# Kernel tuning notes

Measured on AMD Instinct MI355X. Metric: run time of the kernel, lower is better.

Reference implementation:

```python
import jax, jax.numpy as jnp
import numpy as np

B, T, D, H = 256, 256, 64, 512  # batch, seq_len, input_dim, hidden_dim


def setup_inputs() -> dict:
    key = jax.random.key(0)
    ks = jax.random.split(key, 12)
    scale = 0.05
    inp = {"x": jax.random.normal(ks[0], (B, T, D), dtype=jnp.float32)}
    in_dims = [D, H, H]
    for i in range(3):
        inp[f"Wx{i}"] = jax.random.normal(ks[1 + 3 * i], (in_dims[i], H), dtype=jnp.float32) * scale
        inp[f"Wh{i}"] = jax.random.normal(ks[2 + 3 * i], (H, H), dtype=jnp.float32) * scale
        inp[f"b{i}"] = jnp.zeros((H,), dtype=jnp.float32)
    inp["Wf"] = jax.random.normal(ks[10], (H, 1), dtype=jnp.float32) * scale
    inp["bf"] = jnp.zeros((1,), dtype=jnp.float32)
    return inp


def _rnn_seq(x, Wx, Wh, b):
    """SimpleRNN with return_sequences=True. x: [B,T,Din] -> [B,T,H].
    Keras eval mode: dropout inactive. h_t = tanh(x_t Wx + h_{t-1} Wh + b)."""
    # Precompute input projection for all steps (one big GEMM).
    xp = jnp.einsum('btd,dh->bth', x, Wx) + b  # [B,T,H]

    def step(h, xt):
        h2 = jnp.tanh(xt + h @ Wh)
        return h2, h2

    h0 = jnp.zeros((x.shape[0], Wh.shape[0]), dtype=x.dtype)
    _, ys = jax.lax.scan(step, h0, jnp.swapaxes(xp, 0, 1))  # ys: [T,B,H]
    return jnp.swapaxes(ys, 0, 1)


def _rnn_last(x, Wx, Wh, b):
    """SimpleRNN with return_sequences=False. x: [B,T,Din] -> [B,H] (final state)."""
    xp = jnp.einsum('btd,dh->bth', x, Wx) + b

    def step(h, xt):
        h2 = jnp.tanh(xt + h @ Wh)
        return h2, None

    h0 = jnp.zeros((x.shape[0], Wh.shape[0]), dtype=x.dtype)
    hT, _ = jax.lax.scan(step, h0, jnp.swapaxes(xp, 0, 1))
    return hT


def reference(x, Wx0, Wh0, b0, Wx1, Wh1, b1, Wx2, Wh2, b2, Wf, bf):
    h = _rnn_seq(x, Wx0, Wh0, b0)   # [B,T,H]
    h = _rnn_seq(h, Wx1, Wh1, b1)   # [B,T,H]
    h = _rnn_last(h, Wx2, Wh2, b2)  # [B,H]
    return h @ Wf + bf              # [B,1]
```

## Files before the change

### kernel.cpp

```cpp
#include <hip/hip_runtime.h>


typedef unsigned short u16;
typedef unsigned int   u32;

typedef __attribute__((ext_vector_type(8))) short short8;
typedef __attribute__((ext_vector_type(4))) float f32x4;
typedef __attribute__((ext_vector_type(4))) int   i32x4;

#define N_B 256
#define N_T 256
#define N_D 64
#define N_H 512
#define LAY 3
#define BG  8
#define CGS 8
#define ROWS 32
#define WCOL 64
#define CNT_TGT 8
#define HSK_TGT 24
#define CPAD 16
#define CNT_LINES (LAY * BG * N_T)
#define CNT_U32   ((CNT_LINES + 2 * BG) * CPAD)
#define SPIN_LIM (1u << 22)

__device__ __forceinline__ u16 f2bf(float f) {
  union { float f; u32 u; } v; v.f = f;
  u32 u = v.u;
  u += 0x7fffu + ((u >> 16) & 1u);
  return (u16)(u >> 16);
}
__device__ __forceinline__ float bf2f(u16 h) {
  union { u32 u; float f; } v; v.u = ((u32)h) << 16;
  return v.f;
}
__device__ __forceinline__ short8 ld8(const u16* p) { return *(const short8*)p; }
__device__ __forceinline__ short8 cvt8(const float* p) {
  short8 r;
#pragma unroll
  for (int j = 0; j < 8; ++j) r[j] = (short)f2bf(p[j]);
  return r;
}
__device__ __forceinline__ short8 as_s8(i32x4 v) {
  union { i32x4 i; short8 s; } u; u.i = v; return u.s;
}
__device__ __forceinline__ float fast_tanh(float x) {
  float xc = fminf(fmaxf(x, -9.f), 9.f);
  float e  = __builtin_amdgcn_exp2f(xc * 2.8853900817779268f);
  return 1.f - 2.f * __builtin_amdgcn_rcpf(e + 1.f);
}
__device__ __forceinline__ u32 rmw_read(u32* p) {
  u32 v, z = 0;
  asm volatile("global_atomic_add %0, %1, %2, off sc0\n\ts_waitcnt vmcnt(0)"
               : "=v"(v) : "v"(p), "v"(z) : "memory");
  return v;
}
__device__ __forceinline__ void poll_cnt(u32* cp, u32 target, bool fast, bool* dead) {
  u32 it = 0;
  for (;;) {
    u32 v = fast ? rmw_read(cp)
                 : __hip_atomic_load(cp, __ATOMIC_RELAXED, __HIP_MEMORY_SCOPE_AGENT);
    if (v >= target) return;
    if (it >= 2) __builtin_amdgcn_s_sleep(1);
    if (++it > SPIN_LIM) { *dead = true; return; }
  }
}
__device__ __forceinline__ void lds_set(volatile u32* f, u32 v) {
  __hip_atomic_store((u32*)f, v, __ATOMIC_RELEASE, __HIP_MEMORY_SCOPE_WORKGROUP);
}
__device__ __forceinline__ void lds_wait(volatile u32* f, u32 want, bool* dead) {
  u32 it = 0;
  while (__hip_atomic_load((u32*)f, __ATOMIC_ACQUIRE, __HIP_MEMORY_SCOPE_WORKGROUP) != want) {
    if (++it > SPIN_LIM) { *dead = true; return; }
  }
}

__device__ __forceinline__ void load_frags16_fast(const u16* p, i32x4 f[16]) {
  asm volatile(
      "global_load_dwordx4 %0, %16, off sc0\n\t"
      "global_load_dwordx4 %1, %16, off offset:64 sc0\n\t"
      "global_load_dwordx4 %2, %16, off offset:128 sc0\n\t"
      "global_load_dwordx4 %3, %16, off offset:192 sc0\n\t"
      "global_load_dwordx4 %4, %16, off offset:256 sc0\n\t"
      "global_load_dwordx4 %5, %16, off offset:320 sc0\n\t"
      "global_load_dwordx4 %6, %16, off offset:384 sc0\n\t"
      "global_load_dwordx4 %7, %16, off offset:448 sc0\n\t"
      "global_load_dwordx4 %8, %16, off offset:512 sc0\n\t"
      "global_load_dwordx4 %9, %16, off offset:576 sc0\n\t"
      "global_load_dwordx4 %10, %16, off offset:640 sc0\n\t"
      "global_load_dwordx4 %11, %16, off offset:704 sc0\n\t"
      "global_load_dwordx4 %12, %16, off offset:768 sc0\n\t"
      "global_load_dwordx4 %13, %16, off offset:832 sc0\n\t"
      "global_load_dwordx4 %14, %16, off offset:896 sc0\n\t"
      "global_load_dwordx4 %15, %16, off offset:960 sc0\n\t"
      "s_waitcnt vmcnt(0)"
      : "=&v"(f[0]), "=&v"(f[1]), "=&v"(f[2]), "=&v"(f[3]),
        "=&v"(f[4]), "=&v"(f[5]), "=&v"(f[6]), "=&v"(f[7]),
        "=&v"(f[8]), "=&v"(f[9]), "=&v"(f[10]), "=&v"(f[11]),
        "=&v"(f[12]), "=&v"(f[13]), "=&v"(f[14]), "=&v"(f[15])
      : "v"(p) : "memory");
}
__device__ __forceinline__ void load_frags16_slow(const u16* p, i32x4 f[16]) {
  asm volatile(
      "global_load_dwordx4 %0, %16, off sc0 sc1\n\t"
      "global_load_dwordx4 %1, %16, off offset:64 sc0 sc1\n\t"
      "global_load_dwordx4 %2, %16, off offset:128 sc0 sc1\n\t"
      "global_load_dwordx4 %3, %16, off offset:192 sc0 sc1\n\t"
      "global_load_dwordx4 %4, %16, off offset:256 sc0 sc1\n\t"
      "global_load_dwordx4 %5, %16, off offset:320 sc0 sc1\n\t"
      "global_load_dwordx4 %6, %16, off offset:384 sc0 sc1\n\t"
      "global_load_dwordx4 %7, %16, off offset:448 sc0 sc1\n\t"
      "global_load_dwordx4 %8, %16, off offset:512 sc0 sc1\n\t"
      "global_load_dwordx4 %9, %16, off offset:576 sc0 sc1\n\t"
      "global_load_dwordx4 %10, %16, off offset:640 sc0 sc1\n\t"
      "global_load_dwordx4 %11, %16, off offset:704 sc0 sc1\n\t"
      "global_load_dwordx4 %12, %16, off offset:768 sc0 sc1\n\t"
      "global_load_dwordx4 %13, %16, off offset:832 sc0 sc1\n\t"
      "global_load_dwordx4 %14, %16, off offset:896 sc0 sc1\n\t"
      "global_load_dwordx4 %15, %16, off offset:960 sc0 sc1\n\t"
      "s_waitcnt vmcnt(0)"
      : "=&v"(f[0]), "=&v"(f[1]), "=&v"(f[2]), "=&v"(f[3]),
        "=&v"(f[4]), "=&v"(f[5]), "=&v"(f[6]), "=&v"(f[7]),
        "=&v"(f[8]), "=&v"(f[9]), "=&v"(f[10]), "=&v"(f[11]),
        "=&v"(f[12]), "=&v"(f[13]), "=&v"(f[14]), "=&v"(f[15])
      : "v"(p) : "memory");
}

#define MFMA16(a, b, c) __builtin_amdgcn_mfma_f32_16x16x32_bf16((a), (b), (c), 0, 0, 0)

__global__ __launch_bounds__(256, 1)
void rnn_pipe(const float* __restrict__ x,
              const float* __restrict__ Wx0, const float* __restrict__ Wh0, const float* __restrict__ b0,
              const float* __restrict__ Wx1, const float* __restrict__ Wh1, const float* __restrict__ b1,
              const float* __restrict__ Wx2, const float* __restrict__ Wh2, const float* __restrict__ b2,
              u16* __restrict__ seq0, u16* __restrict__ seq1, u16* __restrict__ seq2,
              u32* __restrict__ cnt) {
  const int b    = blockIdx.x & 7;
  const int rst  = blockIdx.x >> 3;
  const int layer = rst >> 3;
  const int j    = rst & 7;
  const int tid  = threadIdx.x;
  const int lane = tid & 63;
  const int w    = tid >> 6;
  const int quad = lane >> 4;
  const int l16  = lane & 15;
  const int half = w & 1;
  const bool is_rec = (w < 2);

  const float *Wx, *Wh, *bias; const u16 *in_seq = nullptr; u16 *out_seq;
  if (layer == 0)      { Wx = Wx0; Wh = Wh0; bias = b0; out_seq = seq0; }
  else if (layer == 1) { Wx = Wx1; Wh = Wh1; bias = b1; in_seq = seq0; out_seq = seq1; }
  else                 { Wx = Wx2; Wh = Wh2; bias = b2; in_seq = seq1; out_seq = seq2; }
  const int kin = (layer == 0) ? N_D : N_H;
  u32* cnt_own  = cnt + (size_t)(layer * BG + b) * N_T * CPAD;
  u32* cnt_prev = (layer > 0) ? cnt + (size_t)((layer - 1) * BG + b) * N_T * CPAD : nullptr;
  u32* hsk_arr  = cnt + (size_t)(CNT_LINES + b) * CPAD;
  u32* hsk_msk  = cnt + (size_t)(CNT_LINES + BG + b) * CPAD;

  __shared__ u16   WhT[WCOL][N_H];
  __shared__ u16   WxT[WCOL][N_H];
  __shared__ float Cbuf[2][ROWS][WCOL + 1];
  __shared__ u32   fastsh;
  __shared__ u32   sflags[6];

  u32 xcc;
  asm volatile("s_getreg_b32 %0, hwreg(HW_REG_XCC_ID)" : "=s"(xcc));
  if (tid == 0) {
    __hip_atomic_fetch_or(hsk_msk, 1u << (xcc & 7), __ATOMIC_RELAXED,
                          __HIP_MEMORY_SCOPE_AGENT);
    asm volatile("s_waitcnt vmcnt(0)" ::: "memory");
    __hip_atomic_fetch_add(hsk_arr, 1u, __ATOMIC_RELAXED, __HIP_MEMORY_SCOPE_AGENT);
  }
  if (tid < 6) sflags[tid] = 0;

  for (int e = tid; e < WCOL * N_H; e += 256) {
    int n = e & 63, k = e >> 6;
    WhT[n][(k + 8 * n) & (N_H - 1)] = f2bf(Wh[k * N_H + j * WCOL + n]);
  }
  for (int e = tid; e < WCOL * kin; e += 256) {
    int n = e & 63, k = e >> 6;
    WxT[n][(k + 8 * n) & (kin - 1)] = f2bf(Wx[k * N_H + j * WCOL + n]);
  }
  float bv[4];
#pragma unroll
  for (int n = 0; n < 4; ++n) bv[n] = bias[j * WCOL + n * 16 + l16];

  if (tid == 0) {
    bool f = false;
    u32 it = 0;
    while (rmw_read(hsk_arr) < (u32)HSK_TGT) {
      __builtin_amdgcn_s_sleep(1);
      if (++it > SPIN_LIM) break;
    }
    if (it <= SPIN_LIM) {
      u32 m = rmw_read(hsk_msk);
      f = (m != 0u) && ((m & (m - 1u)) == 0u);
    }
    fastsh = f ? 1u : 0u;
  }
  __syncthreads();
  const bool fast = (fastsh == 1u);

  const int arow = b * ROWS + half * 16 + l16;
  bool dead = false;

  for (int t = 0; t < N_T; ++t) {
    const int par = t & 1;
    f32x4 acc[4] = {{0.f,0.f,0.f,0.f},{0.f,0.f,0.f,0.f},{0.f,0.f,0.f,0.f},{0.f,0.f,0.f,0.f}};

    if (!is_rec) {
      if (layer == 0) {
        const float* xp = x + ((size_t)arow * N_T + t) * N_D + quad * 8;
        short8 f0 = cvt8(xp), f1 = cvt8(xp + 32);
#pragma unroll
        for (int n = 0; n < 4; ++n) {
          int nl = n * 16 + l16;
          acc[n] = MFMA16(f0, ld8(&WxT[nl][(quad * 8 + 8 * nl) & (N_D - 1)]), acc[n]);
          acc[n] = MFMA16(f1, ld8(&WxT[nl][(32 + quad * 8 + 8 * nl) & (N_D - 1)]), acc[n]);
        }
      } else {
        if (half == 0) {
          if (lane == 0) {
            if (!dead) poll_cnt(cnt_prev + (size_t)t * CPAD, CNT_TGT, fast, &dead);
            lds_set(&sflags[2 + par], (u32)(t + 1));
          }
        } else {
          if (lane == 0 && !dead) lds_wait(&sflags[2 + par], (u32)(t + 1), &dead);
        }
        const u16* sp = in_seq + ((size_t)t * N_B + arow) * N_H + quad * 8;
        i32x4 fr[16];
        if (fast) load_frags16_fast(sp, fr);
        else      load_frags16_slow(sp, fr);
#pragma unroll
        for (int kt = 0; kt < 16; ++kt) {
          short8 a = as_s8(fr[kt]);
#pragma unroll
          for (int n = 0; n < 4; ++n) {
            int nl = n * 16 + l16;
            acc[n] = MFMA16(a, ld8(&WxT[nl][(kt * 32 + quad * 8 + 8 * nl) & (N_H - 1)]), acc[n]);
          }
        }
      }
      int rb = half * 16 + quad * 4;
#pragma unroll
      for (int n = 0; n < 4; ++n)
#pragma unroll
        for (int r = 0; r < 4; ++r)
          Cbuf[par][rb + r][n * 16 + l16] = acc[n][r];
    } else {
      if (t > 0) {
        if (half == 0) {
          if (lane == 0) {
            if (!dead) poll_cnt(cnt_own + (size_t)(t - 1) * CPAD, CNT_TGT, fast, &dead);
            lds_set(&sflags[par], (u32)t);
          }
        } else {
          if (lane == 0 && !dead) lds_wait(&sflags[par], (u32)t, &dead);
        }
        const u16* ap = out_seq + ((size_t)(t - 1) * N_B + arow) * N_H + quad * 8;
        i32x4 fr[16];
        if (fast) load_frags16_fast(ap, fr);
        else      load_frags16_slow(ap, fr);
#pragma unroll
        for (int kt = 0; kt < 16; ++kt) {
          short8 a = as_s8(fr[kt]);
#pragma unroll
          for (int n = 0; n < 4; ++n) {
            int nl = n * 16 + l16;
            acc[n] = MFMA16(a, ld8(&WhT[nl][(kt * 32 + quad * 8 + 8 * nl) & (N_H - 1)]), acc[n]);
          }
        }
      }
    }

    __syncthreads();

    if (is_rec) {
      int rb = half * 16 + quad * 4;
      u32 hv[4][4];
#pragma unroll
      for (int n = 0; n < 4; ++n)
#pragma unroll
        for (int r = 0; r < 4; ++r)
          hv[n][r] = (u32)f2bf(fast_tanh(acc[n][r] + Cbuf[par][rb + r][n * 16 + l16] + bv[n]));
      u16* hdst = out_seq + ((size_t)t * N_B + b * ROWS + half * 16 + quad * 4) * N_H
                  + j * WCOL + l16;
      if (fast) {
        asm volatile(
            "global_store_short %0, %1, off sc0\n\t"
            "global_store_short %0, %2, off offset:1024 sc0\n\t"
            "global_store_short %0, %3, off offset:2048 sc0\n\t"
            "global_store_short %0, %4, off offset:3072 sc0\n\t"
            "global_store_short %0, %5, off offset:32 sc0\n\t"
            "global_store_short %0, %6, off offset:1056 sc0\n\t"
            "global_store_short %0, %7, off offset:2080 sc0\n\t"
            "global_store_short %0, %8, off offset:3104 sc0\n\t"
            "global_store_short %0, %9, off offset:64 sc0\n\t"
            "global_store_short %0, %10, off offset:1088 sc0\n\t"
            "global_store_short %0, %11, off offset:2112 sc0\n\t"
            "global_store_short %0, %12, off offset:3136 sc0\n\t"
            "global_store_short %0, %13, off offset:96 sc0\n\t"
            "global_store_short %0, %14, off offset:1120 sc0\n\t"
            "global_store_short %0, %15, off offset:2144 sc0\n\t"
            "global_store_short %0, %16, off offset:3168 sc0"
            :: "v"(hdst),
               "v"(hv[0][0]), "v"(hv[0][1]), "v"(hv[0][2]), "v"(hv[0][3]),
               "v"(hv[1][0]), "v"(hv[1][1]), "v"(hv[1][2]), "v"(hv[1][3]),
               "v"(hv[2][0]), "v"(hv[2][1]), "v"(hv[2][2]), "v"(hv[2][3]),
               "v"(hv[3][0]), "v"(hv[3][1]), "v"(hv[3][2]), "v"(hv[3][3])
            : "memory");
      } else {
        asm volatile(
            "global_store_short %0, %1, off sc0 sc1\n\t"
            "global_store_short %0, %2, off offset:1024 sc0 sc1\n\t"
            "global_store_short %0, %3, off offset:2048 sc0 sc1\n\t"
            "global_store_short %0, %4, off offset:3072 sc0 sc1\n\t"
            "global_store_short %0, %5, off offset:32 sc0 sc1\n\t"
            "global_store_short %0, %6, off offset:1056 sc0 sc1\n\t"
            "global_store_short %0, %7, off offset:2080 sc0 sc1\n\t"
            "global_store_short %0, %8, off offset:3104 sc0 sc1\n\t"
            "global_store_short %0, %9, off offset:64 sc0 sc1\n\t"
            "global_store_short %0, %10, off offset:1088 sc0 sc1\n\t"
            "global_store_short %0, %11, off offset:2112 sc0 sc1\n\t"
            "global_store_short %0, %12, off offset:3136 sc0 sc1\n\t"
            "global_store_short %0, %13, off offset:96 sc0 sc1\n\t"
            "global_store_short %0, %14, off offset:1120 sc0 sc1\n\t"
            "global_store_short %0, %15, off offset:2144 sc0 sc1\n\t"
            "global_store_short %0, %16, off offset:3168 sc0 sc1"
            :: "v"(hdst),
               "v"(hv[0][0]), "v"(hv[0][1]), "v"(hv[0][2]), "v"(hv[0][3]),
               "v"(hv[1][0]), "v"(hv[1][1]), "v"(hv[1][2]), "v"(hv[1][3]),
               "v"(hv[2][0]), "v"(hv[2][1]), "v"(hv[2][2]), "v"(hv[2][3]),
               "v"(hv[3][0]), "v"(hv[3][1]), "v"(hv[3][2]), "v"(hv[3][3])
            : "memory");
      }
      asm volatile("s_waitcnt vmcnt(0)" ::: "memory");
      if (half == 1) {
        if (lane == 0) lds_set(&sflags[4 + par], (u32)(t + 1));
      } else {
        if (lane == 0) {
          if (!dead) lds_wait(&sflags[4 + par], (u32)(t + 1), &dead);
          u32* cp = cnt_own + (size_t)t * CPAD;
          if (fast) {
            u32 one = 1u;
            asm volatile("global_atomic_add %0, %1, off" :: "v"(cp), "v"(one) : "memory");
          } else {
            __hip_atomic_fetch_add(cp, 1u, __ATOMIC_RELAXED, __HIP_MEMORY_SCOPE_AGENT);
          }
        }
      }
    }
  }
}

__global__ void head_kernel(const u16* __restrict__ seq2, const float* __restrict__ Wf,
                            const float* __restrict__ bf, float* __restrict__ out) {
  int b    = blockIdx.x;
  int lane = threadIdx.x;
  const u16* hrow = seq2 + ((size_t)(N_T - 1) * N_B + b) * N_H;
  float s = 0.f;
#pragma unroll
  for (int r = 0; r < N_H / 64; ++r) {
    int idx = lane * 8 + r;
    s += bf2f(hrow[idx]) * Wf[idx];
  }
#pragma unroll
  for (int off = 32; off > 0; off >>= 1) s += __shfl_down(s, off);
  if (lane == 0) out[b] = s + bf[0];
}

extern "C" void kernel_launch(void* const* d_in, const int* in_sizes, int n_in,
                              void* d_out, int out_size, void* d_ws, size_t ws_size,
                              hipStream_t stream) {
  const float* x   = (const float*)d_in[0];
  const float* Wx0 = (const float*)d_in[1];
  const float* Wh0 = (const float*)d_in[2];
  const float* b0  = (const float*)d_in[3];
  const float* Wx1 = (const float*)d_in[4];
  const float* Wh1 = (const float*)d_in[5];
  const float* b1  = (const float*)d_in[6];
  const float* Wx2 = (const float*)d_in[7];
  const float* Wh2 = (const float*)d_in[8];
  const float* b2  = (const float*)d_in[9];
  const float* Wf  = (const float*)d_in[10];
  const float* bf  = (const float*)d_in[11];
  float* out = (float*)d_out;

  const size_t SEQ_BYTES = (size_t)N_T * N_B * N_H * sizeof(u16);
  if (ws_size < 3 * SEQ_BYTES + (size_t)CNT_U32 * sizeof(u32)) return;

  char* ws  = (char*)d_ws;
  u16* seq0 = (u16*)(ws);
  u16* seq1 = (u16*)(ws + SEQ_BYTES);
  u16* seq2 = (u16*)(ws + 2 * SEQ_BYTES);
  u32* cnt  = (u32*)(ws + 3 * SEQ_BYTES);

  (void)hipMemsetAsync(cnt, 0, (size_t)CNT_U32 * sizeof(u32), stream);

  rnn_pipe<<<LAY * BG * CGS, 256, 0, stream>>>(x, Wx0, Wh0, b0, Wx1, Wh1, b1,
                                               Wx2, Wh2, b2, seq0, seq1, seq2,
                                               cnt);
  head_kernel<<<N_B, 64, 0, stream>>>(seq2, Wf, bf, out);
}
```

Before: 1.222 ms.

## Hoist weight fragments into registers and overlap A-fragment loads with MFMAs

Weight B-fragments are loaded from LDS once before the time loop and kept in 64 short8 registers, so the per-step LDS reads of WxT/WhT go away. The global loads of the activation fragments no longer end in a single vmcnt(0) wait. Each MFMA group instead waits only for its own fragment through a graduated s_waitcnt, so math on early k-tiles overlaps the remaining loads on the serial recurrent path. This uses roughly 256 extra VGPRs per thread, which risks register spills under launch_bounds(256,1).

Measured after the change: 1.086 ms. 11.1% less time.

```diff
diff --git a/kernel.cpp b/kernel.cpp
--- a/kernel.cpp
+++ b/kernel.cpp
@@ -75,7 +75,7 @@
   }
 }
 
-__device__ __forceinline__ void load_frags16_fast(const u16* p, i32x4 f[16]) {
+__device__ __forceinline__ void load16_async_fast(const u16* p, i32x4 f[16]) {
   asm volatile(
       "global_load_dwordx4 %0, %16, off sc0\n\t"
       "global_load_dwordx4 %1, %16, off offset:64 sc0\n\t"
@@ -92,15 +92,14 @@
       "global_load_dwordx4 %12, %16, off offset:768 sc0\n\t"
       "global_load_dwordx4 %13, %16, off offset:832 sc0\n\t"
       "global_load_dwordx4 %14, %16, off offset:896 sc0\n\t"
-      "global_load_dwordx4 %15, %16, off offset:960 sc0\n\t"
-      "s_waitcnt vmcnt(0)"
+      "global_load_dwordx4 %15, %16, off offset:960 sc0"
       : "=&v"(f[0]), "=&v"(f[1]), "=&v"(f[2]), "=&v"(f[3]),
         "=&v"(f[4]), "=&v"(f[5]), "=&v"(f[6]), "=&v"(f[7]),
         "=&v"(f[8]), "=&v"(f[9]), "=&v"(f[10]), "=&v"(f[11]),
         "=&v"(f[12]), "=&v"(f[13]), "=&v"(f[14]), "=&v"(f[15])
       : "v"(p) : "memory");
 }
-__device__ __forceinline__ void load_frags16_slow(const u16* p, i32x4 f[16]) {
+__device__ __forceinline__ void load16_async_slow(const u16* p, i32x4 f[16]) {
   asm volatile(
       "global_load_dwordx4 %0, %16, off sc0 sc1\n\t"
       "global_load_dwordx4 %1, %16, off offset:64 sc0 sc1\n\t"
@@ -117,8 +116,7 @@
       "global_load_dwordx4 %12, %16, off offset:768 sc0 sc1\n\t"
       "global_load_dwordx4 %13, %16, off offset:832 sc0 sc1\n\t"
       "global_load_dwordx4 %14, %16, off offset:896 sc0 sc1\n\t"
-      "global_load_dwordx4 %15, %16, off offset:960 sc0 sc1\n\t"
-      "s_waitcnt vmcnt(0)"
+      "global_load_dwordx4 %15, %16, off offset:960 sc0 sc1"
       : "=&v"(f[0]), "=&v"(f[1]), "=&v"(f[2]), "=&v"(f[3]),
         "=&v"(f[4]), "=&v"(f[5]), "=&v"(f[6]), "=&v"(f[7]),
         "=&v"(f[8]), "=&v"(f[9]), "=&v"(f[10]), "=&v"(f[11]),
@@ -127,6 +125,21 @@
 }
 
 #define MFMA16(a, b, c) __builtin_amdgcn_mfma_f32_16x16x32_bf16((a), (b), (c), 0, 0, 0)
+
+#define STEPK(kt, N)                                                        \
+  do {                                                                      \
+    asm volatile("s_waitcnt vmcnt(" #N ")" : "+v"(fr[kt]) :: "memory");     \
+    short8 a_ = as_s8(fr[kt]);                                              \
+    acc[0] = MFMA16(a_, wf[kt][0], acc[0]);                                 \
+    acc[1] = MFMA16(a_, wf[kt][1], acc[1]);                                 \
+    acc[2] = MFMA16(a_, wf[kt][2], acc[2]);                                 \
+    acc[3] = MFMA16(a_, wf[kt][3], acc[3]);                                 \
+  } while (0)
+#define K16_PIPE()                                                          \
+  STEPK(0, 15); STEPK(1, 14); STEPK(2, 13); STEPK(3, 12);                   \
+  STEPK(4, 11); STEPK(5, 10); STEPK(6, 9);  STEPK(7, 8);                    \
+  STEPK(8, 7);  STEPK(9, 6);  STEPK(10, 5); STEPK(11, 4);                   \
+  STEPK(12, 3); STEPK(13, 2); STEPK(14, 1); STEPK(15, 0)
 
 __global__ __launch_bounds__(256, 1)
 void rnn_pipe(const float* __restrict__ x,
@@ -201,6 +214,32 @@
   __syncthreads();
   const bool fast = (fastsh == 1u);
 
+  short8 wf[16][4];
+  if (is_rec) {
+#pragma unroll
+    for (int kt = 0; kt < 16; ++kt)
+#pragma unroll
+      for (int n = 0; n < 4; ++n) {
+        int nl = n * 16 + l16;
+        wf[kt][n] = ld8(&WhT[nl][(kt * 32 + quad * 8 + 8 * nl) & (N_H - 1)]);
+      }
+  } else if (layer == 0) {
+#pragma unroll
+    for (int n = 0; n < 4; ++n) {
+      int nl = n * 16 + l16;
+      wf[0][n] = ld8(&WxT[nl][(quad * 8 + 8 * nl) & (N_D - 1)]);
+      wf[1][n] = ld8(&WxT[nl][(32 + quad * 8 + 8 * nl) & (N_D - 1)]);
+    }
+  } else {
+#pragma unroll
+    for (int kt = 0; kt < 16; ++kt)
+#pragma unroll
+      for (int n = 0; n < 4; ++n) {
+        int nl = n * 16 + l16;
+        wf[kt][n] = ld8(&WxT[nl][(kt * 32 + quad * 8 + 8 * nl) & (N_H - 1)]);
+      }
+  }
+
   const int arow = b * ROWS + half * 16 + l16;
   bool dead = false;
 
@@ -214,9 +253,8 @@
         short8 f0 = cvt8(xp), f1 = cvt8(xp + 32);
 #pragma unroll
         for (int n = 0; n < 4; ++n) {
-          int nl = n * 16 + l16;
-          acc[n] = MFMA16(f0, ld8(&WxT[nl][(quad * 8 + 8 * nl) & (N_D - 1)]), acc[n]);
-          acc[n] = MFMA16(f1, ld8(&WxT[nl][(32 + quad * 8 + 8 * nl) & (N_D - 1)]), acc[n]);
+          acc[n] = MFMA16(f0, wf[0][n], acc[n]);
+          acc[n] = MFMA16(f1, wf[1][n], acc[n]);
         }
       } else {
         if (half == 0) {
@@ -229,17 +267,9 @@
         }
         const u16* sp = in_seq + ((size_t)t * N_B + arow) * N_H + quad * 8;
         i32x4 fr[16];
-        if (fast) load_frags16_fast(sp, fr);
-        else      load_frags16_slow(sp, fr);
-#pragma unroll
-        for (int kt = 0; kt < 16; ++kt) {
-          short8 a = as_s8(fr[kt]);
-#pragma unroll
-          for (int n = 0; n < 4; ++n) {
-            int nl = n * 16 + l16;
-            acc[n] = MFMA16(a, ld8(&WxT[nl][(kt * 32 + quad * 8 + 8 * nl) & (N_H - 1)]), acc[n]);
-          }
-        }
+        if (fast) load16_async_fast(sp, fr);
+        else      load16_async_slow(sp, fr);
+        K16_PIPE();
       }
       int rb = half * 16 + quad * 4;
 #pragma unroll
@@ -259,17 +289,9 @@
         }
         const u16* ap = out_seq + ((size_t)(t - 1) * N_B + arow) * N_H + quad * 8;
         i32x4 fr[16];
-        if (fast) load_frags16_fast(ap, fr);
-        else      load_frags16_slow(ap, fr);
-#pragma unroll
-        for (int kt = 0; kt < 16; ++kt) {
-          short8 a = as_s8(fr[kt]);
-#pragma unroll
-          for (int n = 0; n < 4; ++n) {
-            int nl = n * 16 + l16;
-            acc[n] = MFMA16(a, ld8(&WhT[nl][(kt * 32 + quad * 8 + 8 * nl) & (N_H - 1)]), acc[n]);
-          }
-        }
+        if (fast) load16_async_fast(ap, fr);
+        else      load16_async_slow(ap, fr);
+        K16_PIPE();
       }
     }
 
```
